# Optimization experiments

Hardware: AMD Instinct MI355X
Metric: run time of the kernel (lower is better)

Reference implementation:

```python
import jax, jax.numpy as jnp
import numpy as np

P, A = 32, 4096            # poses, atoms per pose
S = 1_500_000              # bonded-term subgraphs (bonds/angles/torsions)
T = 1_048_576              # hash-table size (power of two)
EPS = 1e-8


def setup_inputs() -> dict:
    rng = np.random.default_rng(0)
    coords = jnp.asarray((rng.standard_normal((P, A, 3)) * 3.0).astype(np.float32))
    # each subgraph is a path of 2, 3, or 4 atoms; -1 pads unused slots
    lengths = rng.integers(2, 5, size=S)
    atoms = rng.integers(0, A, size=(S, 4)).astype(np.int32)
    atoms = np.where(np.arange(4)[None, :] < lengths[:, None], atoms, -1).astype(np.int32)
    pose = rng.integers(0, P, size=S).astype(np.int32)
    uids = rng.integers(0, 2 ** 20, size=(P, A)).astype(np.int32)
    hv = rng.random((T, 3), dtype=np.float32)
    hv[:, 0] = hv[:, 0] * 50.0 + 10.0                 # force constant K
    hv[:, 1] = hv[:, 1] * 3.0                         # equilibrium value x0
    hv[:, 2] = rng.integers(1, 4, size=T).astype(np.float32)  # torsion periodicity
    return {
        "coords": coords,
        "hash_values": jnp.asarray(hv),
        "subgraph_atoms": jnp.asarray(atoms),
        "subgraph_pose": jnp.asarray(pose),
        "atom_unique_ids": jnp.asarray(uids),
    }


def _cartbonded(coords, hash_values, subgraph_atoms, subgraph_pose, atom_unique_ids):
    valid = subgraph_atoms >= 0                                  # [S,4]
    idx = jnp.where(valid, subgraph_atoms, 0)                    # clipped gather idx
    # hash-table parameter lookup keyed on the atom unique ids along the path
    uid = jnp.where(valid, atom_unique_ids[subgraph_pose[:, None], idx], 0)
    key = (jnp.sum(uid.astype(jnp.uint32), axis=1) % jnp.uint32(T)).astype(jnp.int32)
    params = hash_values[key]                                    # [S,3]
    K, x0, period = params[:, 0], params[:, 1], params[:, 2]
    # subgraph atom gather: [S,4,3]
    pts = coords[subgraph_pose[:, None], idx]
    p0, p1, p2, p3 = pts[:, 0], pts[:, 1], pts[:, 2], pts[:, 3]
    # bond (2-atom path): harmonic in length
    d = jnp.sqrt(jnp.sum((p1 - p0) ** 2, -1) + EPS)
    e_bond = K * (d - x0) ** 2
    # angle (3-atom path): harmonic in angle
    u, v = p0 - p1, p2 - p1
    cosang = jnp.sum(u * v, -1) / (
        jnp.sqrt(jnp.sum(u * u, -1) + EPS) * jnp.sqrt(jnp.sum(v * v, -1) + EPS)
    )
    theta = jnp.arccos(jnp.clip(cosang, -0.999999, 0.999999))
    e_angle = K * (theta - x0) ** 2
    # torsion (4-atom path): periodic
    b1, b2, b3 = p1 - p0, p2 - p1, p3 - p2
    n1 = jnp.cross(b1, b2)
    n2 = jnp.cross(b2, b3)
    b2n = b2 / jnp.sqrt(jnp.sum(b2 * b2, -1, keepdims=True) + EPS)
    m1 = jnp.cross(n1, b2n)
    phi = jnp.arctan2(jnp.sum(m1 * n2, -1), jnp.sum(n1 * n2, -1) + EPS)
    e_tors = K * (1.0 + jnp.cos(period * phi - x0))
    # select energy by path length, segment-reduce to per-pose scores
    nv = jnp.sum(valid, axis=1)
    e = jnp.where(nv == 2, e_bond, jnp.where(nv == 3, e_angle, e_tors))
    return jax.ops.segment_sum(e, subgraph_pose, num_segments=P)


def reference(coords, hash_values, subgraph_atoms, subgraph_pose, atom_unique_ids):
    return _cartbonded(coords, hash_values, subgraph_atoms, subgraph_pose, atom_unique_ids)
```

## Files before the change

### kernel.cpp

```cpp
#include <hip/hip_runtime.h>

#define P_POSES   32
#define A_ATOMS   4096
#define T_HASH    1048576
#define EPSF      1e-8f
#define NBKT      256
#define KS        3
#define CHUNK     2048

typedef int   int4v   __attribute__((ext_vector_type(4)));
typedef float float4v __attribute__((ext_vector_type(4)));

__global__ __launch_bounds__(256) void k_init(int* __restrict__ cursor,
                                              float* __restrict__ out, int cap) {
    const int t = threadIdx.x;
    cursor[t] = t * cap;
    if (t < P_POSES) out[t] = 0.0f;
}

__global__ __launch_bounds__(256) void kA_bucket(const int4v* __restrict__ atoms,
                                                 const int*   __restrict__ pose,
                                                 const int*   __restrict__ uids,
                                                 int*         __restrict__ cursor,
                                                 int4v*       __restrict__ rec,
                                                 int S, int cap) {
    __shared__ int4v buf[CHUNK];
    __shared__ unsigned char bkt[CHUNK];
    __shared__ int cnt[NBKT];
    __shared__ int lstart[NBKT];
    __shared__ int gbase[NBKT];
    __shared__ int wsum[4];

    const int tid  = threadIdx.x;
    const int lane = tid & 63;
    cnt[tid] = 0;
    __syncthreads();

    const int s0 = blockIdx.x * CHUNK;
    int4v pk[8]; int bb[8], rr[8]; bool act[8];

    #pragma unroll
    for (int it = 0; it < 8; ++it) {
        const int s = s0 + it * 256 + tid;
        act[it] = s < S;
        if (act[it]) {
            const int4v a = __builtin_nontemporal_load(&atoms[s]);
            const int   p = __builtin_nontemporal_load(&pose[s]);
            const bool v0 = a.x >= 0, v1 = a.y >= 0, v2 = a.z >= 0, v3 = a.w >= 0;
            const int  i0 = v0 ? a.x : 0;
            const int  i1 = v1 ? a.y : 0;
            const int  i2 = v2 ? a.z : 0;
            const int  i3 = v3 ? a.w : 0;
            const int  nv = (int)v0 + (int)v1 + (int)v2 + (int)v3;
            const int* __restrict__ urow = uids + p * A_ATOMS;
            unsigned int key = (v0 ? (unsigned)urow[i0] : 0u)
                             + (v1 ? (unsigned)urow[i1] : 0u)
                             + (v2 ? (unsigned)urow[i2] : 0u)
                             + (v3 ? (unsigned)urow[i3] : 0u);
            key &= (unsigned)(T_HASH - 1);
            const int b = (p << 3) | (int)(key >> 17);
            int4v r;
            r.x = i0 | (i1 << 16);
            r.y = i2 | (i3 << 16);
            r.z = (int)(key | ((unsigned)nv << 20) | ((unsigned)p << 23));
            r.w = 0;
            pk[it] = r; bb[it] = b;
            rr[it] = atomicAdd(&cnt[b], 1);
        }
    }
    __syncthreads();

    {
        const int c = cnt[tid];
        int x = c;
        #pragma unroll
        for (int d = 1; d < 64; d <<= 1) {
            int y = __shfl_up(x, d, 64);
            if (lane >= d) x += y;
        }
        if (lane == 63) wsum[tid >> 6] = x;
        __syncthreads();
        int off = 0;
        const int w = tid >> 6;
        for (int g = 0; g < w; ++g) off += wsum[g];
        lstart[tid] = x - c + off;
        gbase[tid]  = (c > 0) ? atomicAdd(&cursor[tid], c) : 0;
    }
    __syncthreads();

    #pragma unroll
    for (int it = 0; it < 8; ++it) {
        if (act[it]) {
            const int l = lstart[bb[it]] + rr[it];
            buf[l] = pk[it];
            bkt[l] = (unsigned char)bb[it];
        }
    }
    __syncthreads();

    const int n = (S - s0 < CHUNK) ? (S - s0) : CHUNK;
    for (int idx = tid; idx < n; idx += 256) {
        const int b = bkt[idx];
        rec[(size_t)gbase[b] + (idx - lstart[b])] = buf[idx];
    }
}

__global__ __launch_bounds__(256) void kB_score(const float* __restrict__ coords,
                                                const float* __restrict__ hv,
                                                const int*   __restrict__ cursor,
                                                const int4v* __restrict__ rec,
                                                float*       __restrict__ out, int cap) {
    __shared__ float sC[A_ATOMS * 3];

    const int blk   = blockIdx.x;
    const int pose  = (blk >> 3) & 31;
    const int ks    = blk >> 8;
    const int b     = blk & 255;
    const int tid   = threadIdx.x;

    {
        const float4v* src = (const float4v*)(coords + (size_t)pose * (A_ATOMS * 3));
        float4v* dst = (float4v*)sC;
        #pragma unroll 4
        for (int i = tid; i < (A_ATOMS * 3) / 4; i += 256) dst[i] = src[i];
    }
    __syncthreads();

    const int base = b * cap;
    const int end  = cursor[b];
    float esum = 0.0f;

    for (int i = base + ks * 256 + tid; i < end; i += KS * 256) {
        const int4v r = rec[i];
        const int i0 = r.x & 0xFFFF;
        const int i1 = ((unsigned)r.x) >> 16;
        const int i2 = r.y & 0xFFFF;
        const int i3 = ((unsigned)r.y) >> 16;
        const unsigned rz = (unsigned)r.z;
        const unsigned key = rz & (unsigned)(T_HASH - 1);
        const int nv = (int)((rz >> 20) & 7u);

        const float K      = hv[3 * (size_t)key + 0];
        const float x0     = hv[3 * (size_t)key + 1];
        const float period = hv[3 * (size_t)key + 2];

        const float p0x = sC[3*i0+0], p0y = sC[3*i0+1], p0z = sC[3*i0+2];
        const float p1x = sC[3*i1+0], p1y = sC[3*i1+1], p1z = sC[3*i1+2];
        const float p2x = sC[3*i2+0], p2y = sC[3*i2+1], p2z = sC[3*i2+2];
        const float p3x = sC[3*i3+0], p3y = sC[3*i3+1], p3z = sC[3*i3+2];

        const float dbx = p1x - p0x, dby = p1y - p0y, dbz = p1z - p0z;
        const float d  = sqrtf(dbx*dbx + dby*dby + dbz*dbz + EPSF);
        const float db = d - x0;
        const float e_bond = K * db * db;

        const float ux = -dbx, uy = -dby, uz = -dbz;
        const float vx = p2x - p1x, vy = p2y - p1y, vz = p2z - p1z;
        const float uv = ux*vx + uy*vy + uz*vz;
        const float uu = ux*ux + uy*uy + uz*uz;
        const float vv = vx*vx + vy*vy + vz*vz;
        float cosang = uv / (sqrtf(uu + EPSF) * sqrtf(vv + EPSF));
        cosang = fminf(fmaxf(cosang, -0.999999f), 0.999999f);
        const float theta = acosf(cosang);
        const float da = theta - x0;
        const float e_angle = K * da * da;

        const float b2x = vx,  b2y = vy,  b2z = vz;
        const float b3x = p3x - p2x, b3y = p3y - p2y, b3z = p3z - p2z;
        const float n1x = dby*b2z - dbz*b2y;
        const float n1y = dbz*b2x - dbx*b2z;
        const float n1z = dbx*b2y - dby*b2x;
        const float n2x = b2y*b3z - b2z*b3y;
        const float n2y = b2z*b3x - b2x*b3z;
        const float n2z = b2x*b3y - b2y*b3x;
        const float b2inv = 1.0f / sqrtf(b2x*b2x + b2y*b2y + b2z*b2z + EPSF);
        const float bnx = b2x*b2inv, bny = b2y*b2inv, bnz = b2z*b2inv;
        const float m1x = n1y*bnz - n1z*bny;
        const float m1y = n1z*bnx - n1x*bnz;
        const float m1z = n1x*bny - n1y*bnx;
        const float sy = m1x*n2x + m1y*n2y + m1z*n2z;
        const float sx = n1x*n2x + n1y*n2y + n1z*n2z + EPSF;
        const float phi = atan2f(sy, sx);
        const float e_tors = K * (1.0f + cosf(period*phi - x0));

        esum += (nv == 2) ? e_bond : ((nv == 3) ? e_angle : e_tors);
    }

    #pragma unroll
    for (int off = 32; off > 0; off >>= 1) esum += __shfl_down(esum, off, 64);
    if ((tid & 63) == 0 && esum != 0.0f) atomicAdd(&out[pose], esum);
}

__global__ __launch_bounds__(256) void fb_kernel(const float* __restrict__ coords,
                                                 const float* __restrict__ hv,
                                                 const int4v* __restrict__ atoms,
                                                 const int*   __restrict__ pose,
                                                 const int*   __restrict__ uids,
                                                 float* __restrict__ out, int S) {
    __shared__ float bins[P_POSES];
    if (threadIdx.x < P_POSES) bins[threadIdx.x] = 0.0f;
    __syncthreads();
    const int s = blockIdx.x * blockDim.x + threadIdx.x;
    if (s < S) {
        const int4v a = atoms[s];
        const int   p = pose[s];
        const bool v0 = a.x >= 0, v1 = a.y >= 0, v2 = a.z >= 0, v3 = a.w >= 0;
        const int  i0 = v0 ? a.x : 0, i1 = v1 ? a.y : 0, i2 = v2 ? a.z : 0, i3 = v3 ? a.w : 0;
        const int  nv = (int)v0 + (int)v1 + (int)v2 + (int)v3;
        const int* urow = uids + p * A_ATOMS;
        unsigned int key = (v0?(unsigned)urow[i0]:0u) + (v1?(unsigned)urow[i1]:0u)
                         + (v2?(unsigned)urow[i2]:0u) + (v3?(unsigned)urow[i3]:0u);
        key &= (unsigned)(T_HASH - 1);
        const float K = hv[3*key], x0 = hv[3*key+1], period = hv[3*key+2];
        const float* crow = coords + (size_t)p * (A_ATOMS * 3);
        const float p0x=crow[i0*3],p0y=crow[i0*3+1],p0z=crow[i0*3+2];
        const float p1x=crow[i1*3],p1y=crow[i1*3+1],p1z=crow[i1*3+2];
        const float p2x=crow[i2*3],p2y=crow[i2*3+1],p2z=crow[i2*3+2];
        const float p3x=crow[i3*3],p3y=crow[i3*3+1],p3z=crow[i3*3+2];
        const float dbx=p1x-p0x,dby=p1y-p0y,dbz=p1z-p0z;
        const float d=sqrtf(dbx*dbx+dby*dby+dbz*dbz+EPSF);
        const float e_bond=K*(d-x0)*(d-x0);
        const float ux=-dbx,uy=-dby,uz=-dbz;
        const float vx=p2x-p1x,vy=p2y-p1y,vz=p2z-p1z;
        float cosang=(ux*vx+uy*vy+uz*vz)/(sqrtf(ux*ux+uy*uy+uz*uz+EPSF)*sqrtf(vx*vx+vy*vy+vz*vz+EPSF));
        cosang=fminf(fmaxf(cosang,-0.999999f),0.999999f);
        const float th=acosf(cosang);
        const float e_angle=K*(th-x0)*(th-x0);
        const float b3x=p3x-p2x,b3y=p3y-p2y,b3z=p3z-p2z;
        const float n1x=dby*vz-dbz*vy,n1y=dbz*vx-dbx*vz,n1z=dbx*vy-dby*vx;
        const float n2x=vy*b3z-vz*b3y,n2y=vz*b3x-vx*b3z,n2z=vx*b3y-vy*b3x;
        const float bi=1.0f/sqrtf(vx*vx+vy*vy+vz*vz+EPSF);
        const float bnx=vx*bi,bny=vy*bi,bnz=vz*bi;
        const float m1x=n1y*bnz-n1z*bny,m1y=n1z*bnx-n1x*bnz,m1z=n1x*bny-n1y*bnx;
        const float sy=m1x*n2x+m1y*n2y+m1z*n2z;
        const float sx=n1x*n2x+n1y*n2y+n1z*n2z+EPSF;
        const float e_tors=K*(1.0f+cosf(period*atan2f(sy,sx)-x0));
        atomicAdd(&bins[p],(nv==2)?e_bond:((nv==3)?e_angle:e_tors));
    }
    __syncthreads();
    if (threadIdx.x < P_POSES) {
        const float b = bins[threadIdx.x];
        if (b != 0.0f) atomicAdd(&out[threadIdx.x], b);
    }
}

extern "C" void kernel_launch(void* const* d_in, const int* in_sizes, int n_in,
                              void* d_out, int out_size, void* d_ws, size_t ws_size,
                              hipStream_t stream) {
    const float* coords = (const float*)d_in[0];
    const float* hv     = (const float*)d_in[1];
    const int4v* atoms  = (const int4v*)d_in[2];
    const int*   pose   = (const int*)d_in[3];
    const int*   uids   = (const int*)d_in[4];
    float* out = (float*)d_out;
    const int S = in_sizes[3];

    int cap = (int)(((long long)S / NBKT) * 7 / 5);
    cap = (cap + 63) & ~63;

    const size_t need = 4096 + (size_t)NBKT * cap * 16;

    if (ws_size < need) {
        hipMemsetAsync(out, 0, P_POSES * sizeof(float), stream);
        fb_kernel<<<(S + 255) / 256, 256, 0, stream>>>(coords, hv, atoms, pose, uids, out, S);
        return;
    }

    int*   cursor = (int*)d_ws;
    int4v* rec    = (int4v*)((char*)d_ws + 4096);

    k_init<<<1, 256, 0, stream>>>(cursor, out, cap);
    kA_bucket<<<(S + CHUNK - 1) / CHUNK, 256, 0, stream>>>(atoms, pose, uids, cursor, rec, S, cap);
    kB_score<<<NBKT * KS, 256, 0, stream>>>(coords, hv, cursor, rec, out, cap);
}
```

Measured before the change: 83.47 us.

## Use wave-ballot bucket ranking and unroll scoring loop by two

The bucketing kernel drops the shared-memory staging buffer and the block-wide prefix scan. It ranks items within each pose and key-slice bucket using wave ballots over 32 poses and 8 slices, with one LDS atomic per group and a smaller chunk of 1024 items per block. Records are written straight to global memory at their bucket offsets, so the writes are less coalesced than the old staged copy-out. The scoring kernel handles two records per iteration to expose more memory-level parallelism, and the energy math moves into a shared helper.

```diff
diff --git a/kernel.cpp b/kernel.cpp
--- a/kernel.cpp
+++ b/kernel.cpp
@@ -6,7 +6,8 @@
 #define EPSF      1e-8f
 #define NBKT      256
 #define KS        3
-#define CHUNK     2048
+#define ITEMS     4
+#define CHUNK     (256*ITEMS)
 
 typedef int   int4v   __attribute__((ext_vector_type(4)));
 typedef float float4v __attribute__((ext_vector_type(4)));
@@ -18,91 +19,128 @@
     if (t < P_POSES) out[t] = 0.0f;
 }
 
-__global__ __launch_bounds__(256) void kA_bucket(const int4v* __restrict__ atoms,
-                                                 const int*   __restrict__ pose,
-                                                 const int*   __restrict__ uids,
-                                                 int*         __restrict__ cursor,
-                                                 int4v*       __restrict__ rec,
-                                                 int S, int cap) {
-    __shared__ int4v buf[CHUNK];
-    __shared__ unsigned char bkt[CHUNK];
+__global__ __launch_bounds__(256) void kA2_bucket(const int4v* __restrict__ atoms,
+                                                  const int*   __restrict__ pose,
+                                                  const int*   __restrict__ uids,
+                                                  int*         __restrict__ cursor,
+                                                  int4v*       __restrict__ rec,
+                                                  int S, int cap) {
     __shared__ int cnt[NBKT];
-    __shared__ int lstart[NBKT];
     __shared__ int gbase[NBKT];
-    __shared__ int wsum[4];
-
-    const int tid  = threadIdx.x;
-    const int lane = tid & 63;
+    const int tid = threadIdx.x, lane = tid & 63;
     cnt[tid] = 0;
     __syncthreads();
 
     const int s0 = blockIdx.x * CHUNK;
-    int4v pk[8]; int bb[8], rr[8]; bool act[8];
-
-    #pragma unroll
-    for (int it = 0; it < 8; ++it) {
+    bool  act[ITEMS]; int4v a[ITEMS]; int pp[ITEMS];
+
+    #pragma unroll
+    for (int it = 0; it < ITEMS; ++it) {
         const int s = s0 + it * 256 + tid;
         act[it] = s < S;
         if (act[it]) {
-            const int4v a = __builtin_nontemporal_load(&atoms[s]);
-            const int   p = __builtin_nontemporal_load(&pose[s]);
-            const bool v0 = a.x >= 0, v1 = a.y >= 0, v2 = a.z >= 0, v3 = a.w >= 0;
-            const int  i0 = v0 ? a.x : 0;
-            const int  i1 = v1 ? a.y : 0;
-            const int  i2 = v2 ? a.z : 0;
-            const int  i3 = v3 ? a.w : 0;
-            const int  nv = (int)v0 + (int)v1 + (int)v2 + (int)v3;
-            const int* __restrict__ urow = uids + p * A_ATOMS;
-            unsigned int key = (v0 ? (unsigned)urow[i0] : 0u)
-                             + (v1 ? (unsigned)urow[i1] : 0u)
-                             + (v2 ? (unsigned)urow[i2] : 0u)
-                             + (v3 ? (unsigned)urow[i3] : 0u);
-            key &= (unsigned)(T_HASH - 1);
-            const int b = (p << 3) | (int)(key >> 17);
-            int4v r;
-            r.x = i0 | (i1 << 16);
-            r.y = i2 | (i3 << 16);
-            r.z = (int)(key | ((unsigned)nv << 20) | ((unsigned)p << 23));
-            r.w = 0;
-            pk[it] = r; bb[it] = b;
-            rr[it] = atomicAdd(&cnt[b], 1);
+            a[it]  = __builtin_nontemporal_load(&atoms[s]);
+            pp[it] = __builtin_nontemporal_load(&pose[s]);
+        } else { a[it] = (int4v){0,0,0,0}; pp[it] = 255; }
+    }
+
+    int4v rc[ITEMS]; int bk[ITEMS]; int ss[ITEMS];
+    #pragma unroll
+    for (int it = 0; it < ITEMS; ++it) {
+        const int4v aa = a[it];
+        const bool v0 = aa.x >= 0, v1 = aa.y >= 0, v2 = aa.z >= 0, v3 = aa.w >= 0;
+        const int  i0 = v0 ? aa.x : 0;
+        const int  i1 = v1 ? aa.y : 0;
+        const int  i2 = v2 ? aa.z : 0;
+        const int  i3 = v3 ? aa.w : 0;
+        const int  nv = (int)v0 + (int)v1 + (int)v2 + (int)v3;
+        const int  p  = act[it] ? pp[it] : 0;
+        const int* __restrict__ urow = uids + p * A_ATOMS;
+        unsigned key = (v0 ? (unsigned)urow[i0] : 0u)
+                     + (v1 ? (unsigned)urow[i1] : 0u)
+                     + (v2 ? (unsigned)urow[i2] : 0u)
+                     + (v3 ? (unsigned)urow[i3] : 0u);
+        key &= (unsigned)(T_HASH - 1);
+        int4v r;
+        r.x = i0 | (i1 << 16);
+        r.y = i2 | (i3 << 16);
+        r.z = (int)(key | ((unsigned)nv << 20));
+        r.w = 0;
+        rc[it] = r;
+        ss[it] = act[it] ? (int)(key >> 17) : 8;
+        bk[it] = ((pp[it] & 31) << 3) | (ss[it] & 7);
+    }
+
+    int ofs[ITEMS];
+    #pragma unroll
+    for (int it = 0; it < ITEMS; ++it) {
+        unsigned long long pm = 0ull, sm = 0ull;
+        #pragma unroll
+        for (int q = 0; q < 32; ++q) {
+            const unsigned long long m = __ballot(act[it] && pp[it] == q);
+            if (pp[it] == q) pm = m;
         }
-    }
-    __syncthreads();
-
-    {
-        const int c = cnt[tid];
-        int x = c;
         #pragma unroll
-        for (int d = 1; d < 64; d <<= 1) {
-            int y = __shfl_up(x, d, 64);
-            if (lane >= d) x += y;
+        for (int q = 0; q < 8; ++q) {
+            const unsigned long long m = __ballot(act[it] && ss[it] == q);
+            if (ss[it] == q) sm = m;
         }
-        if (lane == 63) wsum[tid >> 6] = x;
-        __syncthreads();
-        int off = 0;
-        const int w = tid >> 6;
-        for (int g = 0; g < w; ++g) off += wsum[g];
-        lstart[tid] = x - c + off;
-        gbase[tid]  = (c > 0) ? atomicAdd(&cursor[tid], c) : 0;
-    }
-    __syncthreads();
-
-    #pragma unroll
-    for (int it = 0; it < 8; ++it) {
-        if (act[it]) {
-            const int l = lstart[bb[it]] + rr[it];
-            buf[l] = pk[it];
-            bkt[l] = (unsigned char)bb[it];
-        }
-    }
-    __syncthreads();
-
-    const int n = (S - s0 < CHUNK) ? (S - s0) : CHUNK;
-    for (int idx = tid; idx < n; idx += 256) {
-        const int b = bkt[idx];
-        rec[(size_t)gbase[b] + (idx - lstart[b])] = buf[idx];
-    }
+        const unsigned long long gm = pm & sm;
+        const int rank = __popcll(gm & ((1ull << lane) - 1ull));
+        const int ldr  = (int)__ffsll((unsigned long long)gm) - 1;
+        int wb = 0;
+        if (act[it] && lane == ldr) wb = atomicAdd(&cnt[bk[it]], __popcll(gm));
+        wb = __shfl(wb, (ldr < 0) ? 0 : ldr, 64);
+        ofs[it] = wb + rank;
+    }
+    __syncthreads();
+
+    { const int c = cnt[tid]; gbase[tid] = c ? atomicAdd(&cursor[tid], c) : 0; }
+    __syncthreads();
+
+    #pragma unroll
+    for (int it = 0; it < ITEMS; ++it)
+        if (act[it]) rec[(size_t)gbase[bk[it]] + ofs[it]] = rc[it];
+}
+
+__device__ __forceinline__ float item_energy(
+    float p0x, float p0y, float p0z, float p1x, float p1y, float p1z,
+    float p2x, float p2y, float p2z, float p3x, float p3y, float p3z,
+    float K, float x0, float period, int nv)
+{
+    const float dbx = p1x - p0x, dby = p1y - p0y, dbz = p1z - p0z;
+    const float d  = sqrtf(dbx*dbx + dby*dby + dbz*dbz + EPSF);
+    const float db = d - x0;
+    const float e_bond = K * db * db;
+
+    const float vx = p2x - p1x, vy = p2y - p1y, vz = p2z - p1z;
+    const float uv = dbx*vx + dby*vy + dbz*vz;
+    const float uu = dbx*dbx + dby*dby + dbz*dbz;
+    const float vv = vx*vx + vy*vy + vz*vz;
+    float cosang = (-uv) / (sqrtf(uu + EPSF) * sqrtf(vv + EPSF));
+    cosang = fminf(fmaxf(cosang, -0.999999f), 0.999999f);
+    const float theta = acosf(cosang);
+    const float da = theta - x0;
+    const float e_angle = K * da * da;
+
+    const float b3x = p3x - p2x, b3y = p3y - p2y, b3z = p3z - p2z;
+    const float n1x = dby*vz - dbz*vy;
+    const float n1y = dbz*vx - dbx*vz;
+    const float n1z = dbx*vy - dby*vx;
+    const float n2x = vy*b3z - vz*b3y;
+    const float n2y = vz*b3x - vx*b3z;
+    const float n2z = vx*b3y - vy*b3x;
+    const float b2inv = 1.0f / sqrtf(vv + EPSF);
+    const float bnx = vx*b2inv, bny = vy*b2inv, bnz = vz*b2inv;
+    const float m1x = n1y*bnz - n1z*bny;
+    const float m1y = n1z*bnx - n1x*bnz;
+    const float m1z = n1x*bny - n1y*bnx;
+    const float sy = m1x*n2x + m1y*n2y + m1z*n2z;
+    const float sx = n1x*n2x + n1y*n2y + n1z*n2z + EPSF;
+    const float phi = atan2f(sy, sx);
+    const float e_tors = K * (1.0f + cosf(period*phi - x0));
+
+    return (nv == 2) ? e_bond : ((nv == 3) ? e_angle : e_tors);
 }
 
 __global__ __launch_bounds__(256) void kB_score(const float* __restrict__ coords,
@@ -112,11 +150,11 @@
                                                 float*       __restrict__ out, int cap) {
     __shared__ float sC[A_ATOMS * 3];
 
-    const int blk   = blockIdx.x;
-    const int pose  = (blk >> 3) & 31;
-    const int ks    = blk >> 8;
-    const int b     = blk & 255;
-    const int tid   = threadIdx.x;
+    const int blk  = blockIdx.x;
+    const int b    = blk & 255;
+    const int ks   = blk >> 8;
+    const int pose = b >> 3;
+    const int tid  = threadIdx.x;
 
     {
         const float4v* src = (const float4v*)(coords + (size_t)pose * (A_ATOMS * 3));
@@ -126,64 +164,49 @@
     }
     __syncthreads();
 
-    const int base = b * cap;
-    const int end  = cursor[b];
+    const int base   = b * cap;
+    const int end    = cursor[b];
+    const int stride = KS * 256;
     float esum = 0.0f;
 
-    for (int i = base + ks * 256 + tid; i < end; i += KS * 256) {
-        const int4v r = rec[i];
-        const int i0 = r.x & 0xFFFF;
-        const int i1 = ((unsigned)r.x) >> 16;
-        const int i2 = r.y & 0xFFFF;
-        const int i3 = ((unsigned)r.y) >> 16;
-        const unsigned rz = (unsigned)r.z;
-        const unsigned key = rz & (unsigned)(T_HASH - 1);
-        const int nv = (int)((rz >> 20) & 7u);
-
-        const float K      = hv[3 * (size_t)key + 0];
-        const float x0     = hv[3 * (size_t)key + 1];
-        const float period = hv[3 * (size_t)key + 2];
-
-        const float p0x = sC[3*i0+0], p0y = sC[3*i0+1], p0z = sC[3*i0+2];
-        const float p1x = sC[3*i1+0], p1y = sC[3*i1+1], p1z = sC[3*i1+2];
-        const float p2x = sC[3*i2+0], p2y = sC[3*i2+1], p2z = sC[3*i2+2];
-        const float p3x = sC[3*i3+0], p3y = sC[3*i3+1], p3z = sC[3*i3+2];
-
-        const float dbx = p1x - p0x, dby = p1y - p0y, dbz = p1z - p0z;
-        const float d  = sqrtf(dbx*dbx + dby*dby + dbz*dbz + EPSF);
-        const float db = d - x0;
-        const float e_bond = K * db * db;
-
-        const float ux = -dbx, uy = -dby, uz = -dbz;
-        const float vx = p2x - p1x, vy = p2y - p1y, vz = p2z - p1z;
-        const float uv = ux*vx + uy*vy + uz*vz;
-        const float uu = ux*ux + uy*uy + uz*uz;
-        const float vv = vx*vx + vy*vy + vz*vz;
-        float cosang = uv / (sqrtf(uu + EPSF) * sqrtf(vv + EPSF));
-        cosang = fminf(fmaxf(cosang, -0.999999f), 0.999999f);
-        const float theta = acosf(cosang);
-        const float da = theta - x0;
-        const float e_angle = K * da * da;
-
-        const float b2x = vx,  b2y = vy,  b2z = vz;
-        const float b3x = p3x - p2x, b3y = p3y - p2y, b3z = p3z - p2z;
-        const float n1x = dby*b2z - dbz*b2y;
-        const float n1y = dbz*b2x - dbx*b2z;
-        const float n1z = dbx*b2y - dby*b2x;
-        const float n2x = b2y*b3z - b2z*b3y;
-        const float n2y = b2z*b3x - b2x*b3z;
-        const float n2z = b2x*b3y - b2y*b3x;
-        const float b2inv = 1.0f / sqrtf(b2x*b2x + b2y*b2y + b2z*b2z + EPSF);
-        const float bnx = b2x*b2inv, bny = b2y*b2inv, bnz = b2z*b2inv;
-        const float m1x = n1y*bnz - n1z*bny;
-        const float m1y = n1z*bnx - n1x*bnz;
-        const float m1z = n1x*bny - n1y*bnx;
-        const float sy = m1x*n2x + m1y*n2y + m1z*n2z;
-        const float sx = n1x*n2x + n1y*n2y + n1z*n2z + EPSF;
-        const float phi = atan2f(sy, sx);
-        const float e_tors = K * (1.0f + cosf(period*phi - x0));
-
-        esum += (nv == 2) ? e_bond : ((nv == 3) ? e_angle : e_tors);
+    for (int i = base + ks * 256 + tid; i < end; i += 2 * stride) {
+        const int  j    = i + stride;
+        const bool has1 = j < end;
+
+        const int4v r0 = rec[i];
+        const int4v r1 = has1 ? rec[j] : r0;
+
+        const int a0i0 = r0.x & 0xFFFF, a0i1 = ((unsigned)r0.x) >> 16;
+        const int a0i2 = r0.y & 0xFFFF, a0i3 = ((unsigned)r0.y) >> 16;
+        const unsigned z0 = (unsigned)r0.z;
+        const unsigned k0 = z0 & (unsigned)(T_HASH - 1);
+        const int nv0 = (int)((z0 >> 20) & 7u);
+
+        const int a1i0 = r1.x & 0xFFFF, a1i1 = ((unsigned)r1.x) >> 16;
+        const int a1i2 = r1.y & 0xFFFF, a1i3 = ((unsigned)r1.y) >> 16;
+        const unsigned z1 = (unsigned)r1.z;
+        const unsigned k1 = z1 & (unsigned)(T_HASH - 1);
+        const int nv1 = (int)((z1 >> 20) & 7u);
+
+        const float K0 = hv[3*(size_t)k0+0], x00 = hv[3*(size_t)k0+1], pr0 = hv[3*(size_t)k0+2];
+        const float K1 = hv[3*(size_t)k1+0], x01 = hv[3*(size_t)k1+1], pr1 = hv[3*(size_t)k1+2];
+
+        const float q0p0x = sC[3*a0i0+0], q0p0y = sC[3*a0i0+1], q0p0z = sC[3*a0i0+2];
+        const float q0p1x = sC[3*a0i1+0], q0p1y = sC[3*a0i1+1], q0p1z = sC[3*a0i1+2];
+        const float q0p2x = sC[3*a0i2+0], q0p2y = sC[3*a0i2+1], q0p2z = sC[3*a0i2+2];
+        const float q0p3x = sC[3*a0i3+0], q0p3y = sC[3*a0i3+1], q0p3z = sC[3*a0i3+2];
+        const float q1p0x = sC[3*a1i0+0], q1p0y = sC[3*a1i0+1], q1p0z = sC[3*a1i0+2];
+        const float q1p1x = sC[3*a1i1+0], q1p1y = sC[3*a1i1+1], q1p1z = sC[3*a1i1+2];
+        const float q1p2x = sC[3*a1i2+0], q1p2y = sC[3*a1i2+1], q1p2z = sC[3*a1i2+2];
+        const float q1p3x = sC[3*a1i3+0], q1p3y = sC[3*a1i3+1], q1p3z = sC[3*a1i3+2];
+
+        const float e0 = item_energy(q0p0x,q0p0y,q0p0z, q0p1x,q0p1y,q0p1z,
+                                     q0p2x,q0p2y,q0p2z, q0p3x,q0p3y,q0p3z,
+                                     K0, x00, pr0, nv0);
+        const float e1 = item_energy(q1p0x,q1p0y,q1p0z, q1p1x,q1p1y,q1p1z,
+                                     q1p2x,q1p2y,q1p2z, q1p3x,q1p3y,q1p3z,
+                                     K1, x01, pr1, nv1);
+        esum += e0 + (has1 ? e1 : 0.0f);
     }
 
     #pragma unroll
@@ -213,34 +236,17 @@
         key &= (unsigned)(T_HASH - 1);
         const float K = hv[3*key], x0 = hv[3*key+1], period = hv[3*key+2];
         const float* crow = coords + (size_t)p * (A_ATOMS * 3);
-        const float p0x=crow[i0*3],p0y=crow[i0*3+1],p0z=crow[i0*3+2];
-        const float p1x=crow[i1*3],p1y=crow[i1*3+1],p1z=crow[i1*3+2];
-        const float p2x=crow[i2*3],p2y=crow[i2*3+1],p2z=crow[i2*3+2];
-        const float p3x=crow[i3*3],p3y=crow[i3*3+1],p3z=crow[i3*3+2];
-        const float dbx=p1x-p0x,dby=p1y-p0y,dbz=p1z-p0z;
-        const float d=sqrtf(dbx*dbx+dby*dby+dbz*dbz+EPSF);
-        const float e_bond=K*(d-x0)*(d-x0);
-        const float ux=-dbx,uy=-dby,uz=-dbz;
-        const float vx=p2x-p1x,vy=p2y-p1y,vz=p2z-p1z;
-        float cosang=(ux*vx+uy*vy+uz*vz)/(sqrtf(ux*ux+uy*uy+uz*uz+EPSF)*sqrtf(vx*vx+vy*vy+vz*vz+EPSF));
-        cosang=fminf(fmaxf(cosang,-0.999999f),0.999999f);
-        const float th=acosf(cosang);
-        const float e_angle=K*(th-x0)*(th-x0);
-        const float b3x=p3x-p2x,b3y=p3y-p2y,b3z=p3z-p2z;
-        const float n1x=dby*vz-dbz*vy,n1y=dbz*vx-dbx*vz,n1z=dbx*vy-dby*vx;
-        const float n2x=vy*b3z-vz*b3y,n2y=vz*b3x-vx*b3z,n2z=vx*b3y-vy*b3x;
-        const float bi=1.0f/sqrtf(vx*vx+vy*vy+vz*vz+EPSF);
-        const float bnx=vx*bi,bny=vy*bi,bnz=vz*bi;
-        const float m1x=n1y*bnz-n1z*bny,m1y=n1z*bnx-n1x*bnz,m1z=n1x*bny-n1y*bnx;
-        const float sy=m1x*n2x+m1y*n2y+m1z*n2z;
-        const float sx=n1x*n2x+n1y*n2y+n1z*n2z+EPSF;
-        const float e_tors=K*(1.0f+cosf(period*atan2f(sy,sx)-x0));
-        atomicAdd(&bins[p],(nv==2)?e_bond:((nv==3)?e_angle:e_tors));
+        const float e = item_energy(crow[i0*3],crow[i0*3+1],crow[i0*3+2],
+                                    crow[i1*3],crow[i1*3+1],crow[i1*3+2],
+                                    crow[i2*3],crow[i2*3+1],crow[i2*3+2],
+                                    crow[i3*3],crow[i3*3+1],crow[i3*3+2],
+                                    K, x0, period, nv);
+        atomicAdd(&bins[p], e);
     }
     __syncthreads();
     if (threadIdx.x < P_POSES) {
-        const float b = bins[threadIdx.x];
-        if (b != 0.0f) atomicAdd(&out[threadIdx.x], b);
+        const float bsum = bins[threadIdx.x];
+        if (bsum != 0.0f) atomicAdd(&out[threadIdx.x], bsum);
     }
 }
 
@@ -270,6 +276,6 @@
     int4v* rec    = (int4v*)((char*)d_ws + 4096);
 
     k_init<<<1, 256, 0, stream>>>(cursor, out, cap);
-    kA_bucket<<<(S + CHUNK - 1) / CHUNK, 256, 0, stream>>>(atoms, pose, uids, cursor, rec, S, cap);
+    kA2_bucket<<<(S + CHUNK - 1) / CHUNK, 256, 0, stream>>>(atoms, pose, uids, cursor, rec, S, cap);
     kB_score<<<NBKT * KS, 256, 0, stream>>>(coords, hv, cursor, rec, out, cap);
 }
```

New measurement: 95.64 us. 14.6% more time.
